# Kernel optimization log

Measured on AMD Instinct MI355X. Metric: run time of the kernel, lower is better.

## Reference

```python
import jax, jax.numpy as jnp
import numpy as np
from jax import lax

K = 3        # KBA kernel size
GC = 4       # channels per group numerator (gc in torch code): g = c // GC
EPS = 1e-6   # LayerNorm2d eps


def conv2d(x, w, b=None, pad=0, groups=1):
    out = lax.conv_general_dilated(x, w, (1, 1), [(pad, pad), (pad, pad)],
                                   dimension_numbers=('NCHW', 'OIHW', 'NCHW'),
                                   feature_group_count=groups)
    return out if b is None else out + b[None, :, None, None]


def layernorm2d(x, w, b):
    mu = jnp.mean(x, axis=1, keepdims=True)
    var = jnp.mean((x - mu) ** 2, axis=1, keepdims=True)
    y = (x - mu) / jnp.sqrt(var + EPS)
    return w[None, :, None, None] * y + b[None, :, None, None]


def kba_fn(x, att, selfb, selfw):
    # x: (B,c,H,W) features; att: (B,nset,H,W) mixing coeffs
    B, c, H, W = x.shape
    nset = att.shape[1]
    g = c // GC; cg = GC; KK = K * K
    a = att.reshape(B, nset, H * W).transpose(0, 2, 1)              # (B,HW,nset)
    bias = a @ selfb[0]                                             # (B,HW,c)
    attk = (a @ selfw[0]).reshape(B, H * W, g, cg, cg * KK)         # per-pixel kernels
    pad = K // 2
    xp = jnp.pad(x, ((0, 0), (0, 0), (pad, pad), (pad, pad)))
    # im2col / unfold, channel-major then kernel position (matches torch unfold)
    patches = jnp.stack([xp[:, :, i:i + H, j:j + W] for i in range(K) for j in range(K)], axis=2)  # (B,c,KK,H,W)
    uf = patches.reshape(B, g, cg * KK, H * W).transpose(0, 3, 1, 2)  # (B,HW,g,cg*KK)
    out = jnp.einsum('bpgij,bpgj->bpgi', attk, uf).reshape(B, H * W, c) + bias
    return out.transpose(0, 2, 1).reshape(B, c, H, W)


def petformer(x, n1w, n1b, n2w, n2b,
              kdw1, kdw2, kc1a, kc1b, kproj,
              c2a_w, c2a_b, c2b_w, c2b_b, c211_w, c211_b,
              kw, kb, attgamma, ga1,
              temp, qkv_w, qkv_dw_w, mproj_w,
              ca1_w, ca1_b, ca2_w, ca2_b):
    B, C, H, W = x.shape
    # channel attention: global avg pool + 1x1 conv
    gap = jnp.mean(x, axis=(2, 3), keepdims=True)
    ca1 = conv2d(gap, ca1_w, ca1_b)
    ca2 = conv2d(gap, ca2_w, ca2_b)

    # ---- KBA branch ----
    xn = layernorm2d(x, n1w, n1b)
    hid = kdw1.shape[0]
    x1 = conv2d(conv2d(xn, kdw1), kdw2, pad=1, groups=hid)          # dwconv path
    interc = c2a_w.shape[0]
    a = conv2d(xn, c2a_w, c2a_b, pad=1, groups=interc)              # grouped 3x3
    a1, a2 = jnp.split(a, 2, axis=1)                                # SimpleGate
    a = conv2d(a1 * a2, c2b_w, c2b_b)                               # 1x1 -> nset
    att = a * attgamma + conv2d(xn, c211_w, c211_b)
    uf = conv2d(conv2d(xn, kc1a), kc1b, pad=1, groups=hid)          # conv1 path
    x2 = kba_fn(uf, att, kb, kw) * ga1 + uf
    kba_out = conv2d(jax.nn.gelu(x1, approximate=False) * x2, kproj)

    # ---- MDTA branch (transposed channel attention) ----
    xm = layernorm2d(x, n2w, n2b)
    qkv = conv2d(conv2d(xm, qkv_w), qkv_dw_w, pad=1, groups=3 * C)
    q, k, v = jnp.split(qkv, 3, axis=1)
    heads = temp.shape[0]
    _h = lambda t: t.reshape(B, heads, C // heads, H * W)
    q, k, v = _h(q), _h(k), _h(v)
    q = q / jnp.maximum(jnp.linalg.norm(q, axis=-1, keepdims=True), 1e-12)
    k = k / jnp.maximum(jnp.linalg.norm(k, axis=-1, keepdims=True), 1e-12)
    attn = jax.nn.softmax(jnp.einsum('bhcp,bhdp->bhcd', q, k) * temp, axis=-1)
    out = jnp.einsum('bhcd,bhdp->bhcp', attn, v).reshape(B, C, H, W)
    mdta_out = conv2d(out, mproj_w)

    return x + kba_out * ca1 + mdta_out * ca2


def setup_inputs() -> dict:
    key = jax.random.key(0)
    ks = iter(jax.random.split(key, 40))
    nrm = lambda shape, s=0.1: (jax.random.normal(next(ks), shape) * s).astype(jnp.float32)
    B, C, H, W = 4, 48, 64, 64
    HID, NSET, HEADS, INTERC = 96, 32, 8, 24
    return {
        'x': jax.random.normal(next(ks), (B, C, H, W), jnp.float32),
        'n1w': jnp.ones((C,), jnp.float32), 'n1b': jnp.zeros((C,), jnp.float32),
        'n2w': jnp.ones((C,), jnp.float32), 'n2b': jnp.zeros((C,), jnp.float32),
        'kdw1': nrm((HID, C, 1, 1)), 'kdw2': nrm((HID, 1, 3, 3)),
        'kc1a': nrm((HID, C, 1, 1)), 'kc1b': nrm((HID, 1, 3, 3)),
        'kproj': nrm((C, HID, 1, 1)),
        'c2a_w': nrm((INTERC, C // INTERC, 3, 3)), 'c2a_b': jnp.zeros((INTERC,), jnp.float32),
        'c2b_w': nrm((NSET, INTERC // 2, 1, 1)), 'c2b_b': jnp.zeros((NSET,), jnp.float32),
        'c211_w': nrm((NSET, C, 1, 1)), 'c211_b': jnp.zeros((NSET,), jnp.float32),
        'kw': nrm((1, NSET, HID * GC * K * K), 0.02), 'kb': nrm((1, NSET, HID), 0.02),
        'attgamma': jnp.full((1, NSET, 1, 1), 0.01, jnp.float32),
        'ga1': jnp.full((1, HID, 1, 1), 0.01, jnp.float32),
        'temp': jnp.ones((HEADS, 1, 1), jnp.float32),
        'qkv_w': nrm((3 * C, C, 1, 1)), 'qkv_dw_w': nrm((3 * C, 1, 3, 3)),
        'mproj_w': nrm((C, C, 1, 1)),
        'ca1_w': nrm((C, C, 1, 1)), 'ca1_b': jnp.zeros((C,), jnp.float32),
        'ca2_w': nrm((C, C, 1, 1)), 'ca2_b': jnp.zeros((C,), jnp.float32),
    }


def reference(x, n1w, n1b, n2w, n2b,
              kdw1, kdw2, kc1a, kc1b, kproj,
              c2a_w, c2a_b, c2b_w, c2b_b, c211_w, c211_b,
              kw, kb, attgamma, ga1,
              temp, qkv_w, qkv_dw_w, mproj_w,
              ca1_w, ca1_b, ca2_w, ca2_b):
    return petformer(x, n1w, n1b, n2w, n2b, kdw1, kdw2, kc1a, kc1b, kproj,
                     c2a_w, c2a_b, c2b_w, c2b_b, c211_w, c211_b,
                     kw, kb, attgamma, ga1, temp, qkv_w, qkv_dw_w, mproj_w,
                     ca1_w, ca1_b, ca2_w, ca2_b)
```

## Files before the change

### kernel.cpp

```cpp
#include <hip/hip_runtime.h>
#include <hip/hip_bf16.h>
#include <cstdint>

typedef unsigned short ushortT;
typedef __attribute__((ext_vector_type(8))) short short8;
typedef __attribute__((ext_vector_type(4))) float f32x4;

static constexpr int Bn = 4, Cc = 48, Hh = 64, Wd = 64, HW = 4096;
static constexpr int HID = 96, NSET = 32, INTERC = 24, HEADS = 8, CPH = 6;

static constexpr int FXN   = 0;
static constexpr int FA    = 786432;
static constexpr int FB    = 2359296;
static constexpr int FC    = 3932160;
static constexpr int FD    = 5505024;
static constexpr int FARAW = 7077888;
static constexpr int FATT  = 7471104;
static constexpr int FKBA  = 7995392;
static constexpr int FGAP  = 8781824;
static constexpr int FCA1  = 8782016;
static constexpr int FCA2  = 8782208;
static constexpr int FS    = 8782400;
static constexpr int FW    = 8783552;
static constexpr int FATTB = 8930752;
static constexpr int FWT   = 9192896;
static constexpr int FXNB  = 9254336;
static constexpr int FXMB  = 9778624;
static constexpr int FHBF  = 10302912;
static constexpr int FMDB  = 11089344;
static constexpr int FWPW  = 11613632;
static constexpr int FWQK  = 11620800;
static constexpr int FWKP  = 11625408;
static constexpr int FWMP  = 11627712;

static constexpr int W_N1W=0, W_N1B=48, W_N2W=96, W_N2B=144;
static constexpr int W_KDW1=192, W_KDW2=4800, W_KC1A=5664, W_KC1B=10272;
static constexpr int W_KPROJ=11136, W_C2AW=15744, W_C2AB=16176;
static constexpr int W_C2BW=16200, W_C2BB=16584, W_C211W=16616, W_C211B=18152;
static constexpr int W_KW=18184, W_KB=128776, W_ATTG=131848, W_GA1=131880;
static constexpr int W_TEMP=131976, W_QKVW=131984, W_QKVDW=138896, W_MPROJ=140192;
static constexpr int W_CA1W=142496, W_CA1B=144800, W_CA2W=144848, W_CA2B=147152;

__device__ __forceinline__ float b2f(ushortT u) {
    union { uint32_t i; float f; } v; v.i = ((uint32_t)u) << 16; return v.f;
}
__device__ __forceinline__ ushortT f2b(float f) {
    union { float f; uint32_t i; } v; v.f = f;
    uint32_t i = v.i;
    uint32_t lsb = (i >> 16) & 1u;
    i += 0x7fffu + lsb;
    return (ushortT)(i >> 16);
}
__device__ __forceinline__ int dtype_bf16(const uint32_t* n1w_raw) {
    return n1w_raw[0] == 0x3F803F80u;
}
__device__ __forceinline__ ushortT raw_bf(const void* p, int idx, int fl) {
    return fl ? ((const ushortT*)p)[idx] : f2b(((const float*)p)[idx]);
}

struct ConvPack {
    const void* src[27];
    int dstoff[27];
    int n[27];
};
struct RawW {
    const void* kdw1; const void* kc1a; const void* c211w; const void* qkvw;
    const void* kproj; const void* mproj; const void* kw; const void* kb;
};

__global__ void k_prep(ConvPack p, RawW rw, float* __restrict__ dst,
                       ushortT* __restrict__ Wt, ushortT* __restrict__ Wpw,
                       ushortT* __restrict__ Wqk, ushortT* __restrict__ Wkp,
                       ushortT* __restrict__ Wmp,
                       const void* __restrict__ x, float* __restrict__ gap,
                       const uint32_t* __restrict__ n1w_raw) {
    int fl = dtype_bf16(n1w_raw);
    int y = blockIdx.y;
    if (y < 27) {
        int n = p.n[y];
        for (int i = blockIdx.x * 256 + threadIdx.x; i < n; i += 64 * 256) {
            float v;
            if (fl) v = b2f(((const ushortT*)p.src[y])[i]);
            else    v = ((const float*)p.src[y])[i];
            dst[p.dstoff[y] + i] = v;
        }
    } else if (y == 27) {
        for (int u = blockIdx.x * 256 + threadIdx.x; u < 24 * 160 * 32; u += 64 * 256) {
            int n = u & 31;
            int rest = u >> 5;
            int r = rest % 160;
            int gr = rest / 160;
            ushortT out;
            if (r < 144) {
                int j = r >> 2, i = r & 3;
                out = raw_bf(rw.kw, n * 3456 + gr * 144 + i * 36 + j, fl);
            } else if (r < 148) {
                out = raw_bf(rw.kb, n * HID + gr * 4 + (r - 144), fl);
            } else out = 0;
            Wt[u] = out;
        }
    } else if (y == 28) {
        for (int u = blockIdx.x * 256 + threadIdx.x; u < 224 * 64; u += 64 * 256) {
            int co = u >> 6, c = u & 63;
            ushortT v = 0;
            if (c < 48) {
                if (co < 96)       v = raw_bf(rw.kdw1,  co * 48 + c, fl);
                else if (co < 192) v = raw_bf(rw.kc1a,  (co - 96) * 48 + c, fl);
                else               v = raw_bf(rw.c211w, (co - 192) * 48 + c, fl);
            }
            Wpw[u] = v;
        }
    } else if (y == 29) {
        for (int u = blockIdx.x * 256 + threadIdx.x; u < 144 * 64; u += 64 * 256) {
            int co = u >> 6, c = u & 63;
            Wqk[u] = (c < 48) ? raw_bf(rw.qkvw, co * 48 + c, fl) : (ushortT)0;
        }
    } else if (y == 30) {
        for (int u = blockIdx.x * 256 + threadIdx.x; u < 48 * 96; u += 64 * 256) {
            int co = u / 96, c = u % 96;
            Wkp[u] = raw_bf(rw.kproj, co * 96 + c, fl);
        }
    } else if (y == 31) {
        for (int u = blockIdx.x * 256 + threadIdx.x; u < 48 * 64; u += 64 * 256) {
            int co = u >> 6, c = u & 63;
            Wmp[u] = (c < 48) ? raw_bf(rw.mproj, co * 48 + c, fl) : (ushortT)0;
        }
    } else {
        __shared__ float red[4];
        for (int bc = blockIdx.x; bc < Bn * Cc; bc += 64) {
            float s = 0.f;
            if (fl) {
                const ushortT* xb = (const ushortT*)x + bc * HW;
                for (int i = threadIdx.x; i < HW; i += 256) s += b2f(xb[i]);
            } else {
                const float* xb = (const float*)x + bc * HW;
                for (int i = threadIdx.x; i < HW; i += 256) s += xb[i];
            }
            #pragma unroll
            for (int o = 32; o > 0; o >>= 1) s += __shfl_down(s, o);
            int lane = threadIdx.x & 63, wv = threadIdx.x >> 6;
            if (lane == 0) red[wv] = s;
            __syncthreads();
            if (threadIdx.x == 0)
                gap[bc] = (red[0] + red[1] + red[2] + red[3]) * (1.f / HW);
            __syncthreads();
        }
    }
}

__global__ void __launch_bounds__(64) k_ln(const void* __restrict__ x, const uint32_t* __restrict__ n1w_raw,
                     const float* __restrict__ wts, float* __restrict__ xn,
                     ushortT* __restrict__ xnb, ushortT* __restrict__ xmb) {
    int fl = dtype_bf16(n1w_raw);
    int p = blockIdx.x * 64 + threadIdx.x;
    int b = p >> 12, hw = p & 4095;
    float xr[Cc];
    if (fl) {
        const ushortT* xb = (const ushortT*)x + b * Cc * HW + hw;
        #pragma unroll
        for (int c = 0; c < Cc; c++) xr[c] = b2f(xb[c * HW]);
    } else {
        const float* xb = (const float*)x + b * Cc * HW + hw;
        #pragma unroll
        for (int c = 0; c < Cc; c++) xr[c] = xb[c * HW];
    }
    float s = 0.f, ss = 0.f;
    #pragma unroll
    for (int c = 0; c < Cc; c++) { s += xr[c]; ss += xr[c] * xr[c]; }
    float mu = s * (1.f / Cc);
    float var = ss * (1.f / Cc) - mu * mu;
    float r = rsqrtf(var + 1e-6f);
    uint32_t pn[32], pm[32];
    #pragma unroll
    for (int i = 0; i < 24; i++) {
        float y0 = (xr[2 * i] - mu) * r, y1 = (xr[2 * i + 1] - mu) * r;
        float n0 = wts[W_N1W + 2 * i] * y0 + wts[W_N1B + 2 * i];
        float n1 = wts[W_N1W + 2 * i + 1] * y1 + wts[W_N1B + 2 * i + 1];
        float m0 = wts[W_N2W + 2 * i] * y0 + wts[W_N2B + 2 * i];
        float m1 = wts[W_N2W + 2 * i + 1] * y1 + wts[W_N2B + 2 * i + 1];
        xn[(b * Cc + 2 * i) * HW + hw] = n0;
        xn[(b * Cc + 2 * i + 1) * HW + hw] = n1;
        pn[i] = (uint32_t)f2b(n0) | ((uint32_t)f2b(n1) << 16);
        pm[i] = (uint32_t)f2b(m0) | ((uint32_t)f2b(m1) << 16);
    }
    #pragma unroll
    for (int i = 24; i < 32; i++) { pn[i] = 0; pm[i] = 0; }
    uint4* dn = (uint4*)(xnb + (size_t)p * 64);
    uint4* dm = (uint4*)(xmb + (size_t)p * 64);
    #pragma unroll
    for (int qd = 0; qd < 8; qd++) {
        uint4 v; v.x = pn[qd*4]; v.y = pn[qd*4+1]; v.z = pn[qd*4+2]; v.w = pn[qd*4+3];
        dn[qd] = v;
        uint4 u; u.x = pm[qd*4]; u.y = pm[qd*4+1]; u.z = pm[qd*4+2]; u.w = pm[qd*4+3];
        dm[qd] = u;
    }
}

__global__ void __launch_bounds__(256) k_pw1m(const ushortT* __restrict__ xnb, const ushortT* __restrict__ Wpw,
                       const float* __restrict__ wts, float* __restrict__ t1,
                       float* __restrict__ t2, float* __restrict__ attn_t) {
    int wave = threadIdx.x >> 6, lane = threadIdx.x & 63;
    int m = lane & 15, q = lane >> 4;
    int p = blockIdx.x * 64 + wave * 16 + m;
    int b = p >> 12, hw = p & 4095;
    short8 B0 = *(const short8*)(xnb + (size_t)p * 64 + q * 8);
    short8 B1 = *(const short8*)(xnb + (size_t)p * 64 + 32 + q * 8);
    #pragma unroll
    for (int t = 0; t < 14; t++) {
        short8 A0 = *(const short8*)(Wpw + (16 * t + m) * 64 + q * 8);
        short8 A1 = *(const short8*)(Wpw + (16 * t + m) * 64 + 32 + q * 8);
        f32x4 z = {0.f, 0.f, 0.f, 0.f};
        f32x4 D = __builtin_amdgcn_mfma_f32_16x16x32_bf16(A0, B0, z, 0, 0, 0);
        D = __builtin_amdgcn_mfma_f32_16x16x32_bf16(A1, B1, D, 0, 0, 0);
        #pragma unroll
        for (int g = 0; g < 4; g++) {
            int co = 16 * t + 4 * q + g;
            if (t < 6) t1[(b * HID + co) * HW + hw] = D[g];
            else if (t < 12) t2[(b * HID + (co - 96)) * HW + hw] = D[g];
            else {
                int n = co - 192;
                attn_t[(size_t)p * 32 + n] = D[g] + wts[W_C211B + n];
            }
        }
    }
}

__global__ void __launch_bounds__(256) k_dw(const float* __restrict__ t1, const float* __restrict__ t2,
                     const float* __restrict__ xn, const float* __restrict__ wts,
                     float* __restrict__ x1g, float* __restrict__ uf, float* __restrict__ araw) {
    int y = blockIdx.y;
    int pbase = blockIdx.x * 1024 + threadIdx.x * 4;
    int b = pbase >> 12, hw = pbase & 4095, h = hw >> 6, w0 = hw & 63;

    if (y < 192) {
        int c = (y < 96) ? y : y - 96;
        const float* base = (y < 96) ? t1 : t2;
        const float* wk = wts + ((y < 96) ? W_KDW2 : W_KC1B) + c * 9;
        const float* plane = base + (b * HID + c) * HW;

        float a0 = 0.f, a1 = 0.f, a2 = 0.f, a3 = 0.f;
        #pragma unroll
        for (int ki = 0; ki < 3; ki++) {
            int hh = h + ki - 1;
            if ((unsigned)hh < 64u) {
                const float* row = plane + hh * 64 + w0;
                float4 mm = *(const float4*)row;
                float lf = (w0 > 0) ? row[-1] : 0.f;
                float rt = (w0 < 60) ? row[4] : 0.f;
                float k0 = wk[ki * 3], k1 = wk[ki * 3 + 1], k2 = wk[ki * 3 + 2];
                a0 += k0 * lf   + k1 * mm.x + k2 * mm.y;
                a1 += k0 * mm.x + k1 * mm.y + k2 * mm.z;
                a2 += k0 * mm.y + k1 * mm.z + k2 * mm.w;
                a3 += k0 * mm.z + k1 * mm.w + k2 * rt;
            }
        }
        int idx = (b * HID + c) * HW + hw;
        if (y < 96) {
            float4 g;
            g.x = 0.5f * a0 * (1.f + erff(a0 * 0.70710678118654752f));
            g.y = 0.5f * a1 * (1.f + erff(a1 * 0.70710678118654752f));
            g.z = 0.5f * a2 * (1.f + erff(a2 * 0.70710678118654752f));
            g.w = 0.5f * a3 * (1.f + erff(a3 * 0.70710678118654752f));
            *(float4*)(x1g + idx) = g;
        } else {
            float4 o; o.x = a0; o.y = a1; o.z = a2; o.w = a3;
            *(float4*)(uf + idx) = o;
        }
    } else {
        int o = y - 192;
        float bias = wts[W_C2AB + o];
        float a0 = bias, a1 = bias, a2 = bias, a3 = bias;
        #pragma unroll
        for (int ic = 0; ic < 2; ic++) {
            const float* plane = xn + (b * Cc + 2 * o + ic) * HW;
            const float* wk = wts + W_C2AW + (o * 2 + ic) * 9;
            #pragma unroll
            for (int ki = 0; ki < 3; ki++) {
                int hh = h + ki - 1;
                if ((unsigned)hh < 64u) {
                    const float* row = plane + hh * 64 + w0;
                    float4 mm = *(const float4*)row;
                    float lf = (w0 > 0) ? row[-1] : 0.f;
                    float rt = (w0 < 60) ? row[4] : 0.f;
                    float k0 = wk[ki * 3], k1 = wk[ki * 3 + 1], k2 = wk[ki * 3 + 2];
                    a0 += k0 * lf   + k1 * mm.x + k2 * mm.y;
                    a1 += k0 * mm.x + k1 * mm.y + k2 * mm.z;
                    a2 += k0 * mm.y + k1 * mm.z + k2 * mm.w;
                    a3 += k0 * mm.z + k1 * mm.w + k2 * rt;
                }
            }
        }
        float4 out; out.x = a0; out.y = a1; out.z = a2; out.w = a3;
        *(float4*)(araw + (b * INTERC + o) * HW + hw) = out;
    }
}

__global__ void __launch_bounds__(256) k_att(const float* __restrict__ araw, const float* __restrict__ attn_t,
                     const float* __restrict__ wts, ushortT* __restrict__ att_bf) {
    int p = blockIdx.x * 256 + threadIdx.x;
    int b = p >> 12, hw = p & 4095;
    const float* ab = araw + b * INTERC * HW + hw;
    float sg[12];
    #pragma unroll
    for (int i = 0; i < 12; i++) sg[i] = ab[i * HW] * ab[(12 + i) * HW];
    const float* ct = attn_t + (size_t)p * 32;
    uint32_t packed[16];
    #pragma unroll
    for (int nq = 0; nq < 16; nq++) {
        float v2[2];
        #pragma unroll
        for (int u = 0; u < 2; u++) {
            int n = nq * 2 + u;
            float a = wts[W_C2BB + n];
            #pragma unroll
            for (int c = 0; c < 12; c++) a += wts[W_C2BW + n * 12 + c] * sg[c];
            v2[u] = wts[W_ATTG + n] * a + ct[n];
        }
        packed[nq] = (uint32_t)f2b(v2[0]) | ((uint32_t)f2b(v2[1]) << 16);
    }
    uint4* dst = (uint4*)(att_bf + (size_t)p * 32);
    #pragma unroll
    for (int q = 0; q < 4; q++) {
        uint4 v; v.x = packed[q*4]; v.y = packed[q*4+1]; v.z = packed[q*4+2]; v.w = packed[q*4+3];
        dst[q] = v;
    }
}

__global__ void __launch_bounds__(256) k_kba(const ushortT* __restrict__ att_bf, const float* __restrict__ uf,
                     const float* __restrict__ x1g, const ushortT* __restrict__ Wt,
                     const float* __restrict__ wts, ushortT* __restrict__ h_bf) {
    int wave = threadIdx.x >> 6, lane = threadIdx.x & 63;
    int m = lane & 15, q = lane >> 4;
    int gr = blockIdx.y;

    short8 A[10];
    const ushortT* wtg = Wt + gr * 160 * 32;
    #pragma unroll
    for (int t = 0; t < 10; t++)
        A[t] = *(const short8*)(wtg + (16 * t + m) * 32 + q * 8);

    for (int tile = 0; tile < 4; tile++) {
        int p = blockIdx.x * 256 + wave * 64 + tile * 16 + m;
        int b = p >> 12, hw = p & 4095, h = hw >> 6, w = hw & 63;

        short8 Bf = *(const short8*)(att_bf + (size_t)p * 32 + q * 8);

        f32x4 D[10];
        #pragma unroll
        for (int t = 0; t < 10; t++) {
            f32x4 z = {0.f, 0.f, 0.f, 0.f};
            D[t] = __builtin_amdgcn_mfma_f32_16x16x32_bf16(A[t], Bf, z, 0, 0, 0);
        }

        float s0 = 0.f, s1 = 0.f, s2 = 0.f, s3 = 0.f;
        #pragma unroll
        for (int t = 0; t < 9; t++) {
            int j = 4 * t + q;
            int ci = j / 9;
            int kk = j - 9 * ci;
            int ki = kk / 3, kj = kk - 3 * ki;
            int hh = h + ki - 1, ww = w + kj - 1;
            float tap = 0.f;
            if ((unsigned)hh < 64u && (unsigned)ww < 64u)
                tap = uf[(b * HID + gr * 4 + ci) * HW + hh * 64 + ww];
            s0 += D[t][0] * tap;
            s1 += D[t][1] * tap;
            s2 += D[t][2] * tap;
            s3 += D[t][3] * tap;
        }
        s0 += D[9][0]; s1 += D[9][1]; s2 += D[9][2]; s3 += D[9][3];

        s0 += __shfl_xor(s0, 16); s0 += __shfl_xor(s0, 32);
        s1 += __shfl_xor(s1, 16); s1 += __shfl_xor(s1, 32);
        s2 += __shfl_xor(s2, 16); s2 += __shfl_xor(s2, 32);
        s3 += __shfl_xor(s3, 16); s3 += __shfl_xor(s3, 32);

        float sel = (q == 0) ? s0 : ((q == 1) ? s1 : ((q == 2) ? s2 : s3));
        int ch = gr * 4 + q;
        int idx = (b * HID + ch) * HW + hw;
        float x2 = sel * wts[W_GA1 + ch] + uf[idx];
        float hv = x1g[idx] * x2;
        h_bf[(size_t)p * 96 + ch] = f2b(hv);
    }
}

__global__ void __launch_bounds__(256) k_kprojm(const ushortT* __restrict__ h_bf, const ushortT* __restrict__ Wkp,
                        float* __restrict__ kba) {
    int wave = threadIdx.x >> 6, lane = threadIdx.x & 63;
    int m = lane & 15, q = lane >> 4;
    int p = blockIdx.x * 64 + wave * 16 + m;
    int b = p >> 12, hw = p & 4095;
    short8 B0 = *(const short8*)(h_bf + (size_t)p * 96 + q * 8);
    short8 B1 = *(const short8*)(h_bf + (size_t)p * 96 + 32 + q * 8);
    short8 B2 = *(const short8*)(h_bf + (size_t)p * 96 + 64 + q * 8);
    #pragma unroll
    for (int t = 0; t < 3; t++) {
        short8 A0 = *(const short8*)(Wkp + (16 * t + m) * 96 + q * 8);
        short8 A1 = *(const short8*)(Wkp + (16 * t + m) * 96 + 32 + q * 8);
        short8 A2 = *(const short8*)(Wkp + (16 * t + m) * 96 + 64 + q * 8);
        f32x4 z = {0.f, 0.f, 0.f, 0.f};
        f32x4 D = __builtin_amdgcn_mfma_f32_16x16x32_bf16(A0, B0, z, 0, 0, 0);
        D = __builtin_amdgcn_mfma_f32_16x16x32_bf16(A1, B1, D, 0, 0, 0);
        D = __builtin_amdgcn_mfma_f32_16x16x32_bf16(A2, B2, D, 0, 0, 0);
        #pragma unroll
        for (int g = 0; g < 4; g++) {
            int co = 16 * t + 4 * q + g;
            kba[(b * Cc + co) * HW + hw] = D[g];
        }
    }
}

__global__ void __launch_bounds__(256) k_qkvpwm(const ushortT* __restrict__ xmb, const ushortT* __restrict__ Wqk,
                        float* __restrict__ qkvr) {
    int wave = threadIdx.x >> 6, lane = threadIdx.x & 63;
    int m = lane & 15, q = lane >> 4;
    int p = blockIdx.x * 64 + wave * 16 + m;
    int b = p >> 12, hw = p & 4095;
    short8 B0 = *(const short8*)(xmb + (size_t)p * 64 + q * 8);
    short8 B1 = *(const short8*)(xmb + (size_t)p * 64 + 32 + q * 8);
    #pragma unroll
    for (int t = 0; t < 9; t++) {
        short8 A0 = *(const short8*)(Wqk + (16 * t + m) * 64 + q * 8);
        short8 A1 = *(const short8*)(Wqk + (16 * t + m) * 64 + 32 + q * 8);
        f32x4 z = {0.f, 0.f, 0.f, 0.f};
        f32x4 D = __builtin_amdgcn_mfma_f32_16x16x32_bf16(A0, B0, z, 0, 0, 0);
        D = __builtin_amdgcn_mfma_f32_16x16x32_bf16(A1, B1, D, 0, 0, 0);
        #pragma unroll
        for (int g = 0; g < 4; g++) {
            int co = 16 * t + 4 * q + g;
            qkvr[(b * 144 + co) * HW + hw] = D[g];
        }
    }
}

__global__ void __launch_bounds__(256) k_qkvdw(const float* __restrict__ qkvr, const float* __restrict__ wts,
                        float* __restrict__ qkv) {
    int ch = blockIdx.y;
    const float* wk = wts + W_QKVDW + ch * 9;
    int pbase = blockIdx.x * 1024 + threadIdx.x * 4;
    int b = pbase >> 12, hw = pbase & 4095, h = hw >> 6, w0 = hw & 63;
    const float* plane = qkvr + (b * 144 + ch) * HW;

    float a0 = 0.f, a1 = 0.f, a2 = 0.f, a3 = 0.f;
    #pragma unroll
    for (int ki = 0; ki < 3; ki++) {
        int hh = h + ki - 1;
        if ((unsigned)hh < 64u) {
            const float* row = plane + hh * 64 + w0;
            float4 mm = *(const float4*)row;
            float lf = (w0 > 0) ? row[-1] : 0.f;
            float rt = (w0 < 60) ? row[4] : 0.f;
            float k0 = wk[ki * 3], k1 = wk[ki * 3 + 1], k2 = wk[ki * 3 + 2];
            a0 += k0 * lf   + k1 * mm.x + k2 * mm.y;
            a1 += k0 * mm.x + k1 * mm.y + k2 * mm.z;
            a2 += k0 * mm.y + k1 * mm.z + k2 * mm.w;
            a3 += k0 * mm.z + k1 * mm.w + k2 * rt;
        }
    }
    float4 o; o.x = a0; o.y = a1; o.z = a2; o.w = a3;
    *(float4*)(qkv + (b * 144 + ch) * HW + hw) = o;
}

__global__ void k_smat1(const float* __restrict__ qkv, float* __restrict__ Sp) {
    int bh = blockIdx.x, chunk = blockIdx.y;
    int b = bh / HEADS, hd = bh % HEADS;
    const float* qb = qkv + (b * 144 + hd * CPH) * HW;
    const float* kb = qkv + (b * 144 + 48 + hd * CPH) * HW;
    int px = chunk * 256 + threadIdx.x;
    float qv[CPH], kv[CPH];
    #pragma unroll
    for (int c = 0; c < CPH; c++) { qv[c] = qb[c * HW + px]; kv[c] = kb[c * HW + px]; }
    float acc[48];
    #pragma unroll
    for (int c = 0; c < CPH; c++) {
        #pragma unroll
        for (int d = 0; d < CPH; d++) acc[c * CPH + d] = qv[c] * kv[d];
        acc[36 + c] = qv[c] * qv[c];
        acc[42 + c] = kv[c] * kv[c];
    }
    __shared__ float red[48 * 4];
    int lane = threadIdx.x & 63, wv = threadIdx.x >> 6;
    #pragma unroll
    for (int t = 0; t < 48; t++) {
        float v = acc[t];
        #pragma unroll
        for (int o = 32; o > 0; o >>= 1) v += __shfl_down(v, o);
        if (lane == 0) red[t * 4 + wv] = v;
    }
    __syncthreads();
    if (threadIdx.x < 48)
        Sp[(bh * 16 + chunk) * 48 + threadIdx.x] =
            red[threadIdx.x * 4] + red[threadIdx.x * 4 + 1] +
            red[threadIdx.x * 4 + 2] + red[threadIdx.x * 4 + 3];
}

__global__ void k_smat2(const float* __restrict__ Sp, const float* __restrict__ gap,
                        const float* __restrict__ wts, float* __restrict__ S,
                        float* __restrict__ ca1, float* __restrict__ ca2) {
    int bh = blockIdx.x;
    int b = bh / HEADS, hd = bh % HEADS;
    int t = threadIdx.x;
    __shared__ float sm[48];
    if (t < 48) {
        float v = 0.f;
        #pragma unroll
        for (int ch = 0; ch < 16; ch++) v += Sp[(bh * 16 + ch) * 48 + t];
        sm[t] = v;
    }
    __syncthreads();
    if (t < CPH) {
        float rqv = 1.f / fmaxf(sqrtf(sm[36 + t]), 1e-12f);
        float tmp = wts[W_TEMP + hd];
        float row[CPH];
        #pragma unroll
        for (int d = 0; d < CPH; d++) {
            float rkv = 1.f / fmaxf(sqrtf(sm[42 + d]), 1e-12f);
            row[d] = sm[t * CPH + d] * rqv * rkv * tmp;
        }
        float mx = row[0];
        #pragma unroll
        for (int d = 1; d < CPH; d++) mx = fmaxf(mx, row[d]);
        float sum = 0.f;
        #pragma unroll
        for (int d = 0; d < CPH; d++) { row[d] = expf(row[d] - mx); sum += row[d]; }
        float inv = 1.f / sum;
        #pragma unroll
        for (int d = 0; d < CPH; d++) S[bh * 36 + t * CPH + d] = row[d] * inv;
    }
    if (t >= 52 && t < 64) {
        int idx = t - 52;
        int which = idx / 6, cc = idx % 6;
        int co = hd * CPH + cc;
        const float* g = gap + b * Cc;
        float sacc = wts[(which ? W_CA2B : W_CA1B) + co];
        #pragma unroll
        for (int c = 0; c < Cc; c++)
            sacc += wts[(which ? W_CA2W : W_CA1W) + co * Cc + c] * g[c];
        (which ? ca2 : ca1)[b * Cc + co] = sacc;
    }
}

__global__ void __launch_bounds__(256) k_attout(const float* __restrict__ qkv, const float* __restrict__ S,
                         ushortT* __restrict__ mdta_bf) {
    int p = blockIdx.x * 256 + threadIdx.x;
    int b = p >> 12, hw = p & 4095;
    int hd = blockIdx.y;
    const float* vb = qkv + (b * 144 + 96 + hd * CPH) * HW + hw;
    float vv[CPH];
    #pragma unroll
    for (int d = 0; d < CPH; d++) vv[d] = vb[d * HW];
    const float* Sb = S + (b * HEADS + hd) * 36;
    float acc[CPH];
    #pragma unroll
    for (int c = 0; c < CPH; c++) {
        float a = 0.f;
        #pragma unroll
        for (int d = 0; d < CPH; d++) a += Sb[c * CPH + d] * vv[d];
        acc[c] = a;
    }
    uint32_t* dst = (uint32_t*)mdta_bf + (size_t)p * 32 + hd * 3;
    dst[0] = (uint32_t)f2b(acc[0]) | ((uint32_t)f2b(acc[1]) << 16);
    dst[1] = (uint32_t)f2b(acc[2]) | ((uint32_t)f2b(acc[3]) << 16);
    dst[2] = (uint32_t)f2b(acc[4]) | ((uint32_t)f2b(acc[5]) << 16);
    if (hd == 0) {
        uint32_t* pz = (uint32_t*)mdta_bf + (size_t)p * 32 + 24;
        #pragma unroll
        for (int i = 0; i < 8; i++) pz[i] = 0;
    }
}

__global__ void __launch_bounds__(256) k_finalm(const void* __restrict__ x, const uint32_t* __restrict__ n1w_raw,
                        const ushortT* __restrict__ mdta_bf, const ushortT* __restrict__ Wmp,
                        const float* __restrict__ kba, const float* __restrict__ ca1,
                        const float* __restrict__ ca2, void* __restrict__ out) {
    int fl = dtype_bf16(n1w_raw);
    int wave = threadIdx.x >> 6, lane = threadIdx.x & 63;
    int m = lane & 15, q = lane >> 4;
    int p = blockIdx.x * 64 + wave * 16 + m;
    int b = p >> 12, hw = p & 4095;
    short8 B0 = *(const short8*)(mdta_bf + (size_t)p * 64 + q * 8);
    short8 B1 = *(const short8*)(mdta_bf + (size_t)p * 64 + 32 + q * 8);
    #pragma unroll
    for (int t = 0; t < 3; t++) {
        short8 A0 = *(const short8*)(Wmp + (16 * t + m) * 64 + q * 8);
        short8 A1 = *(const short8*)(Wmp + (16 * t + m) * 64 + 32 + q * 8);
        f32x4 z = {0.f, 0.f, 0.f, 0.f};
        f32x4 D = __builtin_amdgcn_mfma_f32_16x16x32_bf16(A0, B0, z, 0, 0, 0);
        D = __builtin_amdgcn_mfma_f32_16x16x32_bf16(A1, B1, D, 0, 0, 0);
        #pragma unroll
        for (int g = 0; g < 4; g++) {
            int co = 16 * t + 4 * q + g;
            int idx = (b * Cc + co) * HW + hw;
            float xv = fl ? b2f(((const ushortT*)x)[idx]) : ((const float*)x)[idx];
            float res = xv + kba[idx] * ca1[b * Cc + co] + D[g] * ca2[b * Cc + co];
            if (fl) ((ushortT*)out)[idx] = f2b(res);
            else    ((float*)out)[idx] = res;
        }
    }
}

extern "C" void kernel_launch(void* const* d_in, const int* in_sizes, int n_in,
                              void* d_out, int out_size, void* d_ws, size_t ws_size,
                              hipStream_t stream) {
    float* ws_f = (float*)d_ws;

    float* xn    = ws_f + FXN;
    float* bufA  = ws_f + FA;
    float* bufB  = ws_f + FB;
    float* bufC  = ws_f + FC;
    float* bufD  = ws_f + FD;
    float* araw  = ws_f + FARAW;
    float* attn_t= ws_f + FATT;
    float* kba   = ws_f + FKBA;
    float* gap   = ws_f + FGAP;
    float* ca1   = ws_f + FCA1;
    float* ca2   = ws_f + FCA2;
    float* Smat  = ws_f + FS;
    float* wts   = ws_f + FW;
    ushortT* att_bf  = (ushortT*)(ws_f + FATTB);
    ushortT* Wt      = (ushortT*)(ws_f + FWT);
    ushortT* xnb     = (ushortT*)(ws_f + FXNB);
    ushortT* xmb     = (ushortT*)(ws_f + FXMB);
    ushortT* h_bf    = (ushortT*)(ws_f + FHBF);
    ushortT* mdta_bf = (ushortT*)(ws_f + FMDB);
    ushortT* Wpw     = (ushortT*)(ws_f + FWPW);
    ushortT* Wqk     = (ushortT*)(ws_f + FWQK);
    ushortT* Wkp     = (ushortT*)(ws_f + FWKP);
    ushortT* Wmp     = (ushortT*)(ws_f + FWMP);

    float* qkvr = bufA;
    float* qkv  = bufC;
    float* Sp   = bufA;
    const uint32_t* n1w_raw = (const uint32_t*)d_in[1];

    static const int wsizes[27] = {48,48,48,48,4608,864,4608,864,4608,432,24,384,32,
                                   1536,32,110592,3072,32,96,8,6912,1296,2304,2304,48,2304,48};
    static const int woffs[27] = {W_N1W,W_N1B,W_N2W,W_N2B,W_KDW1,W_KDW2,W_KC1A,W_KC1B,
                                  W_KPROJ,W_C2AW,W_C2AB,W_C2BW,W_C2BB,W_C211W,W_C211B,
                                  W_KW,W_KB,W_ATTG,W_GA1,W_TEMP,W_QKVW,W_QKVDW,W_MPROJ,
                                  W_CA1W,W_CA1B,W_CA2W,W_CA2B};
    ConvPack cp;
    for (int i = 0; i < 27; i++) {
        cp.src[i] = d_in[i + 1];
        cp.dstoff[i] = woffs[i];
        cp.n[i] = wsizes[i];
    }
    RawW rw;
    rw.kdw1 = d_in[5]; rw.kc1a = d_in[7]; rw.c211w = d_in[14]; rw.qkvw = d_in[21];
    rw.kproj = d_in[9]; rw.mproj = d_in[23]; rw.kw = d_in[16]; rw.kb = d_in[17];

    k_prep<<<dim3(64, 33), 256, 0, stream>>>(cp, rw, wts, Wt, Wpw, Wqk, Wkp, Wmp,
                                             d_in[0], gap, n1w_raw);
    k_ln<<<dim3(256), 64, 0, stream>>>(d_in[0], n1w_raw, wts, xn, xnb, xmb);
    k_pw1m<<<dim3(256), 256, 0, stream>>>(xnb, Wpw, wts, bufA, bufB, attn_t);
    k_dw<<<dim3(16, 216), 256, 0, stream>>>(bufA, bufB, xn, wts, bufC, bufD, araw);
    k_att<<<dim3(64), 256, 0, stream>>>(araw, attn_t, wts, att_bf);
    k_kba<<<dim3(64, 24), 256, 0, stream>>>(att_bf, bufD, bufC, Wt, wts, h_bf);
    k_kprojm<<<dim3(256), 256, 0, stream>>>(h_bf, Wkp, kba);
    k_qkvpwm<<<dim3(256), 256, 0, stream>>>(xmb, Wqk, qkvr);
    k_qkvdw<<<dim3(16, 144), 256, 0, stream>>>(qkvr, wts, qkv);
    k_smat1<<<dim3(32, 16), 256, 0, stream>>>(qkv, Sp);
    k_smat2<<<dim3(32), 64, 0, stream>>>(Sp, gap, wts, Smat, ca1, ca2);
    k_attout<<<dim3(64, 8), 256, 0, stream>>>(qkv, Smat, mdta_bf);
    k_finalm<<<dim3(256), 256, 0, stream>>>(d_in[0], n1w_raw, mdta_bf, Wmp,
                                            kba, ca1, ca2, d_out);
}
```

Measured before the change: 225.4 us.

## Fuse LayerNorm into prep, qkv pointwise into pw1, and attention output into final kernel

Moves the LayerNorm pass into an extra slice of the prep kernel, which reads the norm weights straight from the raw inputs. The qkv pointwise matmul is merged into the first pointwise MFMA kernel, and the KBA projection and attention-value product are folded into the final kernel, so the kba and mdta intermediates are no longer written and re-read. The per-head softmax and channel-attention step runs in the last block of smat1, found with an atomic counter and threadfence, which removes that separate launch. Overall this drops five launches and several global round trips, at the cost of heavier final and pw1 kernels and strided fp32 v reads in the final kernel.

```diff
diff --git a/kernel.cpp b/kernel.cpp
--- a/kernel.cpp
+++ b/kernel.cpp
@@ -16,7 +16,6 @@
 static constexpr int FD    = 5505024;
 static constexpr int FARAW = 7077888;
 static constexpr int FATT  = 7471104;
-static constexpr int FKBA  = 7995392;
 static constexpr int FGAP  = 8781824;
 static constexpr int FCA1  = 8782016;
 static constexpr int FCA2  = 8782208;
@@ -27,11 +26,12 @@
 static constexpr int FXNB  = 9254336;
 static constexpr int FXMB  = 9778624;
 static constexpr int FHBF  = 10302912;
-static constexpr int FMDB  = 11089344;
-static constexpr int FWPW  = 11613632;
-static constexpr int FWQK  = 11620800;
-static constexpr int FWKP  = 11625408;
-static constexpr int FWMP  = 11627712;
+static constexpr int FWPW  = 11089344;
+static constexpr int FWQK  = 11096512;
+static constexpr int FWKP  = 11101120;
+static constexpr int FWMP  = 11103424;
+static constexpr int FCNT  = 11104960;
+static constexpr int FQKVR = 11105024;
 
 static constexpr int W_N1W=0, W_N1B=48, W_N2W=96, W_N2B=144;
 static constexpr int W_KDW1=192, W_KDW2=4800, W_KC1A=5664, W_KC1B=10272;
@@ -56,6 +56,9 @@
 }
 __device__ __forceinline__ ushortT raw_bf(const void* p, int idx, int fl) {
     return fl ? ((const ushortT*)p)[idx] : f2b(((const float*)p)[idx]);
+}
+__device__ __forceinline__ float raw_f(const void* p, int idx, int fl) {
+    return fl ? b2f(((const ushortT*)p)[idx]) : ((const float*)p)[idx];
 }
 
 struct ConvPack {
@@ -66,6 +69,7 @@
 struct RawW {
     const void* kdw1; const void* kc1a; const void* c211w; const void* qkvw;
     const void* kproj; const void* mproj; const void* kw; const void* kb;
+    const void* n1w; const void* n1b; const void* n2w; const void* n2b;
 };
 
 __global__ void k_prep(ConvPack p, RawW rw, float* __restrict__ dst,
@@ -73,16 +77,15 @@
                        ushortT* __restrict__ Wqk, ushortT* __restrict__ Wkp,
                        ushortT* __restrict__ Wmp,
                        const void* __restrict__ x, float* __restrict__ gap,
+                       float* __restrict__ xn, ushortT* __restrict__ xnb,
+                       ushortT* __restrict__ xmb, unsigned* __restrict__ cnt,
                        const uint32_t* __restrict__ n1w_raw) {
     int fl = dtype_bf16(n1w_raw);
     int y = blockIdx.y;
     if (y < 27) {
         int n = p.n[y];
         for (int i = blockIdx.x * 256 + threadIdx.x; i < n; i += 64 * 256) {
-            float v;
-            if (fl) v = b2f(((const ushortT*)p.src[y])[i]);
-            else    v = ((const float*)p.src[y])[i];
-            dst[p.dstoff[y] + i] = v;
+            dst[p.dstoff[y] + i] = raw_f(p.src[y], i, fl);
         }
     } else if (y == 27) {
         for (int u = blockIdx.x * 256 + threadIdx.x; u < 24 * 160 * 32; u += 64 * 256) {
@@ -125,7 +128,8 @@
             int co = u >> 6, c = u & 63;
             Wmp[u] = (c < 48) ? raw_bf(rw.mproj, co * 48 + c, fl) : (ushortT)0;
         }
-    } else {
+    } else if (y == 32) {
+        if (blockIdx.x == 0 && threadIdx.x == 0) cnt[0] = 0u;
         __shared__ float red[4];
         for (int bc = blockIdx.x; bc < Bn * Cc; bc += 64) {
             float s = 0.f;
@@ -145,60 +149,57 @@
                 gap[bc] = (red[0] + red[1] + red[2] + red[3]) * (1.f / HW);
             __syncthreads();
         }
-    }
-}
-
-__global__ void __launch_bounds__(64) k_ln(const void* __restrict__ x, const uint32_t* __restrict__ n1w_raw,
-                     const float* __restrict__ wts, float* __restrict__ xn,
-                     ushortT* __restrict__ xnb, ushortT* __restrict__ xmb) {
-    int fl = dtype_bf16(n1w_raw);
-    int p = blockIdx.x * 64 + threadIdx.x;
-    int b = p >> 12, hw = p & 4095;
-    float xr[Cc];
-    if (fl) {
-        const ushortT* xb = (const ushortT*)x + b * Cc * HW + hw;
-        #pragma unroll
-        for (int c = 0; c < Cc; c++) xr[c] = b2f(xb[c * HW]);
     } else {
-        const float* xb = (const float*)x + b * Cc * HW + hw;
-        #pragma unroll
-        for (int c = 0; c < Cc; c++) xr[c] = xb[c * HW];
-    }
-    float s = 0.f, ss = 0.f;
-    #pragma unroll
-    for (int c = 0; c < Cc; c++) { s += xr[c]; ss += xr[c] * xr[c]; }
-    float mu = s * (1.f / Cc);
-    float var = ss * (1.f / Cc) - mu * mu;
-    float r = rsqrtf(var + 1e-6f);
-    uint32_t pn[32], pm[32];
-    #pragma unroll
-    for (int i = 0; i < 24; i++) {
-        float y0 = (xr[2 * i] - mu) * r, y1 = (xr[2 * i + 1] - mu) * r;
-        float n0 = wts[W_N1W + 2 * i] * y0 + wts[W_N1B + 2 * i];
-        float n1 = wts[W_N1W + 2 * i + 1] * y1 + wts[W_N1B + 2 * i + 1];
-        float m0 = wts[W_N2W + 2 * i] * y0 + wts[W_N2B + 2 * i];
-        float m1 = wts[W_N2W + 2 * i + 1] * y1 + wts[W_N2B + 2 * i + 1];
-        xn[(b * Cc + 2 * i) * HW + hw] = n0;
-        xn[(b * Cc + 2 * i + 1) * HW + hw] = n1;
-        pn[i] = (uint32_t)f2b(n0) | ((uint32_t)f2b(n1) << 16);
-        pm[i] = (uint32_t)f2b(m0) | ((uint32_t)f2b(m1) << 16);
-    }
-    #pragma unroll
-    for (int i = 24; i < 32; i++) { pn[i] = 0; pm[i] = 0; }
-    uint4* dn = (uint4*)(xnb + (size_t)p * 64);
-    uint4* dm = (uint4*)(xmb + (size_t)p * 64);
-    #pragma unroll
-    for (int qd = 0; qd < 8; qd++) {
-        uint4 v; v.x = pn[qd*4]; v.y = pn[qd*4+1]; v.z = pn[qd*4+2]; v.w = pn[qd*4+3];
-        dn[qd] = v;
-        uint4 u; u.x = pm[qd*4]; u.y = pm[qd*4+1]; u.z = pm[qd*4+2]; u.w = pm[qd*4+3];
-        dm[qd] = u;
-    }
-}
-
-__global__ void __launch_bounds__(256) k_pw1m(const ushortT* __restrict__ xnb, const ushortT* __restrict__ Wpw,
+        int pp = blockIdx.x * 256 + threadIdx.x;
+        int b = pp >> 12, hw = pp & 4095;
+        float xr[Cc];
+        if (fl) {
+            const ushortT* xb = (const ushortT*)x + b * Cc * HW + hw;
+            #pragma unroll
+            for (int c = 0; c < Cc; c++) xr[c] = b2f(xb[c * HW]);
+        } else {
+            const float* xb = (const float*)x + b * Cc * HW + hw;
+            #pragma unroll
+            for (int c = 0; c < Cc; c++) xr[c] = xb[c * HW];
+        }
+        float s = 0.f, ss = 0.f;
+        #pragma unroll
+        for (int c = 0; c < Cc; c++) { s += xr[c]; ss += xr[c] * xr[c]; }
+        float mu = s * (1.f / Cc);
+        float var = ss * (1.f / Cc) - mu * mu;
+        float r = rsqrtf(var + 1e-6f);
+        uint32_t pn[32], pm[32];
+        #pragma unroll
+        for (int i = 0; i < 24; i++) {
+            float y0 = (xr[2 * i] - mu) * r, y1 = (xr[2 * i + 1] - mu) * r;
+            float n0 = raw_f(rw.n1w, 2 * i, fl) * y0 + raw_f(rw.n1b, 2 * i, fl);
+            float n1 = raw_f(rw.n1w, 2 * i + 1, fl) * y1 + raw_f(rw.n1b, 2 * i + 1, fl);
+            float m0 = raw_f(rw.n2w, 2 * i, fl) * y0 + raw_f(rw.n2b, 2 * i, fl);
+            float m1 = raw_f(rw.n2w, 2 * i + 1, fl) * y1 + raw_f(rw.n2b, 2 * i + 1, fl);
+            xn[(b * Cc + 2 * i) * HW + hw] = n0;
+            xn[(b * Cc + 2 * i + 1) * HW + hw] = n1;
+            pn[i] = (uint32_t)f2b(n0) | ((uint32_t)f2b(n1) << 16);
+            pm[i] = (uint32_t)f2b(m0) | ((uint32_t)f2b(m1) << 16);
+        }
+        #pragma unroll
+        for (int i = 24; i < 32; i++) { pn[i] = 0; pm[i] = 0; }
+        uint4* dn = (uint4*)(xnb + (size_t)pp * 64);
+        uint4* dm = (uint4*)(xmb + (size_t)pp * 64);
+        #pragma unroll
+        for (int qd = 0; qd < 8; qd++) {
+            uint4 v; v.x = pn[qd*4]; v.y = pn[qd*4+1]; v.z = pn[qd*4+2]; v.w = pn[qd*4+3];
+            dn[qd] = v;
+            uint4 u; u.x = pm[qd*4]; u.y = pm[qd*4+1]; u.z = pm[qd*4+2]; u.w = pm[qd*4+3];
+            dm[qd] = u;
+        }
+    }
+}
+
+__global__ void __launch_bounds__(256) k_pw1m(const ushortT* __restrict__ xnb, const ushortT* __restrict__ xmb,
+                       const ushortT* __restrict__ Wpw, const ushortT* __restrict__ Wqk,
                        const float* __restrict__ wts, float* __restrict__ t1,
-                       float* __restrict__ t2, float* __restrict__ attn_t) {
+                       float* __restrict__ t2, float* __restrict__ attn_t,
+                       float* __restrict__ qkvr) {
     int wave = threadIdx.x >> 6, lane = threadIdx.x & 63;
     int m = lane & 15, q = lane >> 4;
     int p = blockIdx.x * 64 + wave * 16 + m;
@@ -221,6 +222,21 @@
                 int n = co - 192;
                 attn_t[(size_t)p * 32 + n] = D[g] + wts[W_C211B + n];
             }
+        }
+    }
+    short8 C0 = *(const short8*)(xmb + (size_t)p * 64 + q * 8);
+    short8 C1 = *(const short8*)(xmb + (size_t)p * 64 + 32 + q * 8);
+    #pragma unroll
+    for (int t = 0; t < 9; t++) {
+        short8 A0 = *(const short8*)(Wqk + (16 * t + m) * 64 + q * 8);
+        short8 A1 = *(const short8*)(Wqk + (16 * t + m) * 64 + 32 + q * 8);
+        f32x4 z = {0.f, 0.f, 0.f, 0.f};
+        f32x4 D = __builtin_amdgcn_mfma_f32_16x16x32_bf16(A0, C0, z, 0, 0, 0);
+        D = __builtin_amdgcn_mfma_f32_16x16x32_bf16(A1, C1, D, 0, 0, 0);
+        #pragma unroll
+        for (int g = 0; g < 4; g++) {
+            int co = 16 * t + 4 * q + g;
+            qkvr[(b * 144 + co) * HW + hw] = D[g];
         }
     }
 }
@@ -384,55 +400,6 @@
     }
 }
 
-__global__ void __launch_bounds__(256) k_kprojm(const ushortT* __restrict__ h_bf, const ushortT* __restrict__ Wkp,
-                        float* __restrict__ kba) {
-    int wave = threadIdx.x >> 6, lane = threadIdx.x & 63;
-    int m = lane & 15, q = lane >> 4;
-    int p = blockIdx.x * 64 + wave * 16 + m;
-    int b = p >> 12, hw = p & 4095;
-    short8 B0 = *(const short8*)(h_bf + (size_t)p * 96 + q * 8);
-    short8 B1 = *(const short8*)(h_bf + (size_t)p * 96 + 32 + q * 8);
-    short8 B2 = *(const short8*)(h_bf + (size_t)p * 96 + 64 + q * 8);
-    #pragma unroll
-    for (int t = 0; t < 3; t++) {
-        short8 A0 = *(const short8*)(Wkp + (16 * t + m) * 96 + q * 8);
-        short8 A1 = *(const short8*)(Wkp + (16 * t + m) * 96 + 32 + q * 8);
-        short8 A2 = *(const short8*)(Wkp + (16 * t + m) * 96 + 64 + q * 8);
-        f32x4 z = {0.f, 0.f, 0.f, 0.f};
-        f32x4 D = __builtin_amdgcn_mfma_f32_16x16x32_bf16(A0, B0, z, 0, 0, 0);
-        D = __builtin_amdgcn_mfma_f32_16x16x32_bf16(A1, B1, D, 0, 0, 0);
-        D = __builtin_amdgcn_mfma_f32_16x16x32_bf16(A2, B2, D, 0, 0, 0);
-        #pragma unroll
-        for (int g = 0; g < 4; g++) {
-            int co = 16 * t + 4 * q + g;
-            kba[(b * Cc + co) * HW + hw] = D[g];
-        }
-    }
-}
-
-__global__ void __launch_bounds__(256) k_qkvpwm(const ushortT* __restrict__ xmb, const ushortT* __restrict__ Wqk,
-                        float* __restrict__ qkvr) {
-    int wave = threadIdx.x >> 6, lane = threadIdx.x & 63;
-    int m = lane & 15, q = lane >> 4;
-    int p = blockIdx.x * 64 + wave * 16 + m;
-    int b = p >> 12, hw = p & 4095;
-    short8 B0 = *(const short8*)(xmb + (size_t)p * 64 + q * 8);
-    short8 B1 = *(const short8*)(xmb + (size_t)p * 64 + 32 + q * 8);
-    #pragma unroll
-    for (int t = 0; t < 9; t++) {
-        short8 A0 = *(const short8*)(Wqk + (16 * t + m) * 64 + q * 8);
-        short8 A1 = *(const short8*)(Wqk + (16 * t + m) * 64 + 32 + q * 8);
-        f32x4 z = {0.f, 0.f, 0.f, 0.f};
-        f32x4 D = __builtin_amdgcn_mfma_f32_16x16x32_bf16(A0, B0, z, 0, 0, 0);
-        D = __builtin_amdgcn_mfma_f32_16x16x32_bf16(A1, B1, D, 0, 0, 0);
-        #pragma unroll
-        for (int g = 0; g < 4; g++) {
-            int co = 16 * t + 4 * q + g;
-            qkvr[(b * 144 + co) * HW + hw] = D[g];
-        }
-    }
-}
-
 __global__ void __launch_bounds__(256) k_qkvdw(const float* __restrict__ qkvr, const float* __restrict__ wts,
                         float* __restrict__ qkv) {
     int ch = blockIdx.y;
@@ -461,7 +428,10 @@
     *(float4*)(qkv + (b * 144 + ch) * HW + hw) = o;
 }
 
-__global__ void k_smat1(const float* __restrict__ qkv, float* __restrict__ Sp) {
+__global__ void k_smat1(const float* __restrict__ qkv, float* __restrict__ Sp,
+                        const float* __restrict__ gap, const float* __restrict__ wts,
+                        float* __restrict__ S, float* __restrict__ ca1,
+                        float* __restrict__ ca2, unsigned* __restrict__ cnt) {
     int bh = blockIdx.x, chunk = blockIdx.y;
     int b = bh / HEADS, hd = bh % HEADS;
     const float* qb = qkv + (b * 144 + hd * CPH) * HW;
@@ -492,30 +462,37 @@
         Sp[(bh * 16 + chunk) * 48 + threadIdx.x] =
             red[threadIdx.x * 4] + red[threadIdx.x * 4 + 1] +
             red[threadIdx.x * 4 + 2] + red[threadIdx.x * 4 + 3];
-}
-
-__global__ void k_smat2(const float* __restrict__ Sp, const float* __restrict__ gap,
-                        const float* __restrict__ wts, float* __restrict__ S,
-                        float* __restrict__ ca1, float* __restrict__ ca2) {
-    int bh = blockIdx.x;
-    int b = bh / HEADS, hd = bh % HEADS;
+    __syncthreads();
+    __shared__ unsigned lastFlag;
+    if (threadIdx.x == 0) {
+        __threadfence();
+        lastFlag = (atomicAdd(cnt, 1u) == 511u) ? 1u : 0u;
+    }
+    __syncthreads();
+    if (lastFlag == 0) return;
+    __threadfence();
+    __shared__ float sm[1536];
+    const volatile float* Sv = Sp;
+    for (int s = threadIdx.x; s < 1536; s += 256) {
+        int sb = s / 48, k = s % 48;
+        float v = 0.f;
+        #pragma unroll
+        for (int ch = 0; ch < 16; ch++) v += Sv[(sb * 16 + ch) * 48 + k];
+        sm[s] = v;
+    }
+    __syncthreads();
     int t = threadIdx.x;
-    __shared__ float sm[48];
-    if (t < 48) {
-        float v = 0.f;
-        #pragma unroll
-        for (int ch = 0; ch < 16; ch++) v += Sp[(bh * 16 + ch) * 48 + t];
-        sm[t] = v;
-    }
-    __syncthreads();
-    if (t < CPH) {
-        float rqv = 1.f / fmaxf(sqrtf(sm[36 + t]), 1e-12f);
-        float tmp = wts[W_TEMP + hd];
+    if (t < 192) {
+        int sbh = t / 6, c = t % 6;
+        int hd2 = sbh % 8;
+        const float* base = sm + sbh * 48;
+        float rqv = 1.f / fmaxf(sqrtf(base[36 + c]), 1e-12f);
+        float tmp = wts[W_TEMP + hd2];
         float row[CPH];
         #pragma unroll
         for (int d = 0; d < CPH; d++) {
-            float rkv = 1.f / fmaxf(sqrtf(sm[42 + d]), 1e-12f);
-            row[d] = sm[t * CPH + d] * rqv * rkv * tmp;
+            float rkv = 1.f / fmaxf(sqrtf(base[42 + d]), 1e-12f);
+            row[d] = base[c * CPH + d] * rqv * rkv * tmp;
         }
         float mx = row[0];
         #pragma unroll
@@ -525,74 +502,88 @@
         for (int d = 0; d < CPH; d++) { row[d] = expf(row[d] - mx); sum += row[d]; }
         float inv = 1.f / sum;
         #pragma unroll
-        for (int d = 0; d < CPH; d++) S[bh * 36 + t * CPH + d] = row[d] * inv;
-    }
-    if (t >= 52 && t < 64) {
-        int idx = t - 52;
-        int which = idx / 6, cc = idx % 6;
-        int co = hd * CPH + cc;
-        const float* g = gap + b * Cc;
+        for (int d = 0; d < CPH; d++) S[sbh * 36 + c * CPH + d] = row[d] * inv;
+    }
+    for (int e = t; e < 384; e += 256) {
+        int which = e / 192, r = e % 192;
+        int b2 = r / 48, co = r % 48;
+        const float* g = gap + b2 * Cc;
         float sacc = wts[(which ? W_CA2B : W_CA1B) + co];
         #pragma unroll
         for (int c = 0; c < Cc; c++)
             sacc += wts[(which ? W_CA2W : W_CA1W) + co * Cc + c] * g[c];
-        (which ? ca2 : ca1)[b * Cc + co] = sacc;
-    }
-}
-
-__global__ void __launch_bounds__(256) k_attout(const float* __restrict__ qkv, const float* __restrict__ S,
-                         ushortT* __restrict__ mdta_bf) {
-    int p = blockIdx.x * 256 + threadIdx.x;
-    int b = p >> 12, hw = p & 4095;
-    int hd = blockIdx.y;
-    const float* vb = qkv + (b * 144 + 96 + hd * CPH) * HW + hw;
-    float vv[CPH];
-    #pragma unroll
-    for (int d = 0; d < CPH; d++) vv[d] = vb[d * HW];
-    const float* Sb = S + (b * HEADS + hd) * 36;
-    float acc[CPH];
-    #pragma unroll
-    for (int c = 0; c < CPH; c++) {
-        float a = 0.f;
-        #pragma unroll
-        for (int d = 0; d < CPH; d++) a += Sb[c * CPH + d] * vv[d];
-        acc[c] = a;
-    }
-    uint32_t* dst = (uint32_t*)mdta_bf + (size_t)p * 32 + hd * 3;
-    dst[0] = (uint32_t)f2b(acc[0]) | ((uint32_t)f2b(acc[1]) << 16);
-    dst[1] = (uint32_t)f2b(acc[2]) | ((uint32_t)f2b(acc[3]) << 16);
-    dst[2] = (uint32_t)f2b(acc[4]) | ((uint32_t)f2b(acc[5]) << 16);
-    if (hd == 0) {
-        uint32_t* pz = (uint32_t*)mdta_bf + (size_t)p * 32 + 24;
-        #pragma unroll
-        for (int i = 0; i < 8; i++) pz[i] = 0;
+        (which ? ca2 : ca1)[b2 * Cc + co] = sacc;
     }
 }
 
 __global__ void __launch_bounds__(256) k_finalm(const void* __restrict__ x, const uint32_t* __restrict__ n1w_raw,
-                        const ushortT* __restrict__ mdta_bf, const ushortT* __restrict__ Wmp,
-                        const float* __restrict__ kba, const float* __restrict__ ca1,
+                        const ushortT* __restrict__ h_bf, const ushortT* __restrict__ Wkp,
+                        const ushortT* __restrict__ Wmp, const float* __restrict__ qkv,
+                        const float* __restrict__ S, const float* __restrict__ ca1,
                         const float* __restrict__ ca2, void* __restrict__ out) {
     int fl = dtype_bf16(n1w_raw);
     int wave = threadIdx.x >> 6, lane = threadIdx.x & 63;
     int m = lane & 15, q = lane >> 4;
     int p = blockIdx.x * 64 + wave * 16 + m;
     int b = p >> 12, hw = p & 4095;
-    short8 B0 = *(const short8*)(mdta_bf + (size_t)p * 64 + q * 8);
-    short8 B1 = *(const short8*)(mdta_bf + (size_t)p * 64 + 32 + q * 8);
+
+    __shared__ float S_l[288];
+    __shared__ float caL[96];
+    for (int i = threadIdx.x; i < 288; i += 256) S_l[i] = S[b * 288 + i];
+    for (int i = threadIdx.x; i < 96; i += 256)
+        caL[i] = (i < 48) ? ca1[b * 48 + i] : ca2[b * 48 + (i - 48)];
+    __syncthreads();
+
+    short8 H0 = *(const short8*)(h_bf + (size_t)p * 96 + q * 8);
+    short8 H1 = *(const short8*)(h_bf + (size_t)p * 96 + 32 + q * 8);
+    short8 H2 = *(const short8*)(h_bf + (size_t)p * 96 + 64 + q * 8);
+    f32x4 Dk[3];
+    #pragma unroll
+    for (int t = 0; t < 3; t++) {
+        short8 A0 = *(const short8*)(Wkp + (16 * t + m) * 96 + q * 8);
+        short8 A1 = *(const short8*)(Wkp + (16 * t + m) * 96 + 32 + q * 8);
+        short8 A2 = *(const short8*)(Wkp + (16 * t + m) * 96 + 64 + q * 8);
+        f32x4 z = {0.f, 0.f, 0.f, 0.f};
+        f32x4 D = __builtin_amdgcn_mfma_f32_16x16x32_bf16(A0, H0, z, 0, 0, 0);
+        D = __builtin_amdgcn_mfma_f32_16x16x32_bf16(A1, H1, D, 0, 0, 0);
+        Dk[t] = __builtin_amdgcn_mfma_f32_16x16x32_bf16(A2, H2, D, 0, 0, 0);
+    }
+
+    const float* vbase = qkv + (b * 144 + 96) * HW + hw;
+    short8 Bm0, Bm1;
+    #pragma unroll
+    for (int jj = 0; jj < 8; jj++) {
+        int c0 = q * 8 + jj;
+        int hd0 = c0 / 6, cc0 = c0 - 6 * hd0;
+        float a = 0.f;
+        #pragma unroll
+        for (int d = 0; d < CPH; d++)
+            a += S_l[hd0 * 36 + cc0 * 6 + d] * vbase[(hd0 * 6 + d) * HW];
+        Bm0[jj] = (short)f2b(a);
+        int c1 = 32 + q * 8 + jj;
+        float bv = 0.f;
+        if (c1 < 48) {
+            int hd1 = c1 / 6, cc1 = c1 - 6 * hd1;
+            #pragma unroll
+            for (int d = 0; d < CPH; d++)
+                bv += S_l[hd1 * 36 + cc1 * 6 + d] * vbase[(hd1 * 6 + d) * HW];
+        }
+        Bm1[jj] = (short)f2b(bv);
+    }
+
     #pragma unroll
     for (int t = 0; t < 3; t++) {
         short8 A0 = *(const short8*)(Wmp + (16 * t + m) * 64 + q * 8);
         short8 A1 = *(const short8*)(Wmp + (16 * t + m) * 64 + 32 + q * 8);
         f32x4 z = {0.f, 0.f, 0.f, 0.f};
-        f32x4 D = __builtin_amdgcn_mfma_f32_16x16x32_bf16(A0, B0, z, 0, 0, 0);
-        D = __builtin_amdgcn_mfma_f32_16x16x32_bf16(A1, B1, D, 0, 0, 0);
+        f32x4 D = __builtin_amdgcn_mfma_f32_16x16x32_bf16(A0, Bm0, z, 0, 0, 0);
+        D = __builtin_amdgcn_mfma_f32_16x16x32_bf16(A1, Bm1, D, 0, 0, 0);
         #pragma unroll
         for (int g = 0; g < 4; g++) {
             int co = 16 * t + 4 * q + g;
             int idx = (b * Cc + co) * HW + hw;
             float xv = fl ? b2f(((const ushortT*)x)[idx]) : ((const float*)x)[idx];
-            float res = xv + kba[idx] * ca1[b * Cc + co] + D[g] * ca2[b * Cc + co];
+            float res = xv + Dk[t][g] * caL[co] + D[g] * caL[48 + co];
             if (fl) ((ushortT*)out)[idx] = f2b(res);
             else    ((float*)out)[idx] = res;
         }
@@ -611,7 +602,6 @@
     float* bufD  = ws_f + FD;
     float* araw  = ws_f + FARAW;
     float* attn_t= ws_f + FATT;
-    float* kba   = ws_f + FKBA;
     float* gap   = ws_f + FGAP;
     float* ca1   = ws_f + FCA1;
     float* ca2   = ws_f + FCA2;
@@ -622,13 +612,13 @@
     ushortT* xnb     = (ushortT*)(ws_f + FXNB);
     ushortT* xmb     = (ushortT*)(ws_f + FXMB);
     ushortT* h_bf    = (ushortT*)(ws_f + FHBF);
-    ushortT* mdta_bf = (ushortT*)(ws_f + FMDB);
     ushortT* Wpw     = (ushortT*)(ws_f + FWPW);
     ushortT* Wqk     = (ushortT*)(ws_f + FWQK);
     ushortT* Wkp     = (ushortT*)(ws_f + FWKP);
     ushortT* Wmp     = (ushortT*)(ws_f + FWMP);
-
-    float* qkvr = bufA;
+    unsigned* cnt    = (unsigned*)(ws_f + FCNT);
+    float* qkvr      = ws_f + FQKVR;
+
     float* qkv  = bufC;
     float* Sp   = bufA;
     const uint32_t* n1w_raw = (const uint32_t*)d_in[1];
@@ -648,20 +638,16 @@
     RawW rw;
     rw.kdw1 = d_in[5]; rw.kc1a = d_in[7]; rw.c211w = d_in[14]; rw.qkvw = d_in[21];
     rw.kproj = d_in[9]; rw.mproj = d_in[23]; rw.kw = d_in[16]; rw.kb = d_in[17];
-
-    k_prep<<<dim3(64, 33), 256, 0, stream>>>(cp, rw, wts, Wt, Wpw, Wqk, Wkp, Wmp,
-                                             d_in[0], gap, n1w_raw);
-    k_ln<<<dim3(256), 64, 0, stream>>>(d_in[0], n1w_raw, wts, xn, xnb, xmb);
-    k_pw1m<<<dim3(256), 256, 0, stream>>>(xnb, Wpw, wts, bufA, bufB, attn_t);
+    rw.n1w = d_in[1]; rw.n1b = d_in[2]; rw.n2w = d_in[3]; rw.n2b = d_in[4];
+
+    k_prep<<<dim3(64, 34), 256, 0, stream>>>(cp, rw, wts, Wt, Wpw, Wqk, Wkp, Wmp,
+                                             d_in[0], gap, xn, xnb, xmb, cnt, n1w_raw);
+    k_pw1m<<<dim3(256), 256, 0, stream>>>(xnb, xmb, Wpw, Wqk, wts, bufA, bufB, attn_t, qkvr);
     k_dw<<<dim3(16, 216), 256, 0, stream>>>(bufA, bufB, xn, wts, bufC, bufD, araw);
     k_att<<<dim3(64), 256, 0, stream>>>(araw, attn_t, wts, att_bf);
     k_kba<<<dim3(64, 24), 256, 0, stream>>>(att_bf, bufD, bufC, Wt, wts, h_bf);
-    k_kprojm<<<dim3(256), 256, 0, stream>>>(h_bf, Wkp, kba);
-    k_qkvpwm<<<dim3(256), 256, 0, stream>>>(xmb, Wqk, qkvr);
     k_qkvdw<<<dim3(16, 144), 256, 0, stream>>>(qkvr, wts, qkv);
-    k_smat1<<<dim3(32, 16), 256, 0, stream>>>(qkv, Sp);
-    k_smat2<<<dim3(32), 64, 0, stream>>>(Sp, gap, wts, Smat, ca1, ca2);
-    k_attout<<<dim3(64, 8), 256, 0, stream>>>(qkv, Smat, mdta_bf);
-    k_finalm<<<dim3(256), 256, 0, stream>>>(d_in[0], n1w_raw, mdta_bf, Wmp,
-                                            kba, ca1, ca2, d_out);
-}
+    k_smat1<<<dim3(32, 16), 256, 0, stream>>>(qkv, Sp, gap, wts, Smat, ca1, ca2, cnt);
+    k_finalm<<<dim3(256), 256, 0, stream>>>(d_in[0], n1w_raw, h_bf, Wkp, Wmp,
+                                            qkv, Smat, ca1, ca2, d_out);
+}
```

New measurement: 270.3 us. 1.2x slower.
